# Performance work log

Measured on AMD Instinct MI355X. Metric: run time of the kernel, lower is better.

The kernel has to match this reference:

```python
import jax, jax.numpy as jnp
import numpy as np

GROUPS = 32
EPS = 1e-5


def setup_inputs() -> dict:
    key = jax.random.key(0)
    ks = jax.random.split(key, 6)
    B, H, W, C = 2, 64, 64, 512
    wscale = 0.02  # keep logits in a sane range for softmax
    return {
        "x": jax.random.normal(ks[0], (B, H, W, C), dtype=jnp.float32),
        "gamma": jnp.ones((C,), jnp.float32),
        "beta": jnp.zeros((C,), jnp.float32),
        "wq": jax.random.normal(ks[1], (C, C), dtype=jnp.float32) * wscale,
        "bq": jnp.zeros((C,), jnp.float32),
        "wk": jax.random.normal(ks[2], (C, C), dtype=jnp.float32) * wscale,
        "bk": jnp.zeros((C,), jnp.float32),
        "wv": jax.random.normal(ks[3], (C, C), dtype=jnp.float32) * wscale,
        "bv": jnp.zeros((C,), jnp.float32),
        "wp": jax.random.normal(ks[4], (C, C), dtype=jnp.float32) * wscale,
        "bp": jnp.zeros((C,), jnp.float32),
    }


def _group_norm(x, gamma, beta):
    B, H, W, C = x.shape
    xg = x.reshape(B, H, W, GROUPS, C // GROUPS)
    mean = xg.mean(axis=(1, 2, 4), keepdims=True)
    var = xg.var(axis=(1, 2, 4), keepdims=True)
    xn = ((xg - mean) * jax.lax.rsqrt(var + EPS)).reshape(B, H, W, C)
    return xn * gamma + beta


def reference(x, gamma, beta, wq, bq, wk, bk, wv, bv, wp, bp):
    B, H, W, C = x.shape
    xn = _group_norm(x, gamma, beta)
    # 1x1 convs == per-pixel linear layers
    q = (xn @ wq + bq).reshape(B, H * W, C)
    k = (xn @ wk + bk).reshape(B, H * W, C)
    v = (xn @ wv + bv).reshape(B, H * W, C)
    scale = C ** (-0.5)
    attn = jax.nn.softmax(jnp.einsum("bqc,bkc->bqk", q, k) * scale, axis=-1)
    out = jnp.einsum("bqk,bkc->bqc", attn, v).reshape(B, H, W, C)
    return (out @ wp + bp) + x
```

## Files before the change

### kernel.cpp

```cpp
#include <hip/hip_runtime.h>


typedef __bf16 bf16_t;
typedef __bf16 bf16x8 __attribute__((ext_vector_type(8)));
typedef __bf16 bf16x4 __attribute__((ext_vector_type(4)));
typedef float  f32x4  __attribute__((ext_vector_type(4)));

__device__ __forceinline__ bf16x8 ld8(const bf16_t* p) {
    return *reinterpret_cast<const bf16x8*>(p);
}
__device__ __forceinline__ f32x4 mfma16(bf16x8 a, bf16x8 b, f32x4 c) {
    return __builtin_amdgcn_mfma_f32_16x16x32_bf16(a, b, c, 0, 0, 0);
}
__device__ __forceinline__ void gload16(const bf16_t* gp, bf16_t* lp) {
    __builtin_amdgcn_global_load_lds(
        (const __attribute__((address_space(1))) void*)gp,
        (__attribute__((address_space(3))) void*)lp, 16, 0, 0);
}

#define NPIX 8192
#define C512 512
#define SEQ  4096
#define QSCALE 0.044194173824159216f

__global__ __launch_bounds__(256) void gn_sum_k(const float* __restrict__ x,
                                                float* __restrict__ accum) {
    int bg    = blockIdx.x >> 3;
    int slice = blockIdx.x & 7;
    int b = bg >> 5, g = bg & 31;
    const float* xp = x + (size_t)b * SEQ * C512 + g * 16;
    float s = 0.f, s2 = 0.f;
    #pragma unroll
    for (int pp = 0; pp < 2; pp++) {
        int p = slice * 512 + pp * 256 + threadIdx.x;
        const float4* q = reinterpret_cast<const float4*>(xp + (size_t)p * C512);
        #pragma unroll
        for (int i = 0; i < 4; i++) {
            float4 v = q[i];
            s  += v.x + v.y + v.z + v.w;
            s2 += v.x*v.x + v.y*v.y + v.z*v.z + v.w*v.w;
        }
    }
    #pragma unroll
    for (int off = 32; off >= 1; off >>= 1) {
        s  += __shfl_down(s, off);
        s2 += __shfl_down(s2, off);
    }
    __shared__ float rs[4], rs2[4];
    int wave = threadIdx.x >> 6;
    if ((threadIdx.x & 63) == 0) { rs[wave] = s; rs2[wave] = s2; }
    __syncthreads();
    if (threadIdx.x == 0) {
        float S = rs[0] + rs[1] + rs[2] + rs[3];
        float S2 = rs2[0] + rs2[1] + rs2[2] + rs2[3];
        atomicAdd(&accum[bg * 2],     S);
        atomicAdd(&accum[bg * 2 + 1], S2);
    }
}

__global__ __launch_bounds__(256) void wt_conv_k(const float* wq, const float* wk,
                                                 const float* wv, const float* wp,
                                                 const float* bq, const float* bk,
                                                 const float* bv,
                                                 bf16_t* wqkvT, bf16_t* wpT,
                                                 float* bqkv) {
    int y = blockIdx.y;
    if (y == 4) {
        if (blockIdx.x >= 6) return;
        int i = blockIdx.x * 256 + threadIdx.x;
        float v = (i < 512) ? bq[i] * QSCALE : (i < 1024) ? bk[i - 512] : bv[i - 1024];
        bqkv[i] = v;
        return;
    }
    const float* w = (y == 0) ? wq : (y == 1) ? wk : (y == 2) ? wv : wp;
    float scale = (y == 0) ? QSCALE : 1.0f;
    int tid = blockIdx.x * 256 + threadIdx.x;
    int n = tid >> 9, k = tid & 511;
    bf16_t val = (bf16_t)(w[(size_t)k * C512 + n] * scale);
    if (y < 3) wqkvT[((size_t)y * C512 + n) * C512 + k] = val;
    else       wpT[(size_t)n * C512 + k] = val;
}

__global__ __launch_bounds__(256) void xn_k(const float* __restrict__ x,
                                            const float* __restrict__ accum,
                                            const float* __restrict__ gamma,
                                            const float* __restrict__ beta,
                                            bf16_t* __restrict__ xn) {
    size_t idx = ((size_t)blockIdx.x * 256 + threadIdx.x) * 4;
    int c = (int)(idx & 511);
    size_t pix = idx >> 9;
    int b = (int)(pix >> 12);
    int g = c >> 4;
    float sum = accum[(b * 32 + g) * 2];
    float ssq = accum[(b * 32 + g) * 2 + 1];
    float mean = sum * (1.f / 65536.f);
    float var  = ssq * (1.f / 65536.f) - mean * mean;
    float rstd = rsqrtf(var + 1e-5f);
    float4 v  = *reinterpret_cast<const float4*>(x + idx);
    float4 gm = *reinterpret_cast<const float4*>(gamma + c);
    float4 bt = *reinterpret_cast<const float4*>(beta + c);
    bf16x4 o;
    o[0] = (bf16_t)((v.x - mean) * rstd * gm.x + bt.x);
    o[1] = (bf16_t)((v.y - mean) * rstd * gm.y + bt.y);
    o[2] = (bf16_t)((v.z - mean) * rstd * gm.z + bt.z);
    o[3] = (bf16_t)((v.w - mean) * rstd * gm.w + bt.w);
    *reinterpret_cast<bf16x4*>(xn + idx) = o;
}

template <int MODE>
__global__ __launch_bounds__(256, 2) void gemm128_k(
        const bf16_t* __restrict__ Aall, const bf16_t* __restrict__ Ball,
        const float* __restrict__ bias, const float* __restrict__ resid,
        void* __restrict__ out0, void* __restrict__ out1,
        void* __restrict__ out2, void* __restrict__ out3,
        float* __restrict__ lsum) {
    constexpr int TM  = (MODE == 3) ? 64 : 128;
    constexpr int ASZ = TM * 32;
    constexpr int ACH = TM / 16;
    constexpr int CPW = (ACH + 8) / 4;
    constexpr int MI  = TM / 32;
    constexpr int SME = (MODE == 0) ? (128 * 136) : (2 * ASZ + 8192);
    __shared__ bf16_t smem[SME];

    int lane = threadIdx.x & 63;
    int w    = threadIdx.x >> 6;
    int wr   = w >> 1, wc = w & 1;
    int lrow = lane & 15, quad = lane >> 4;

    const bf16_t* A  = Aall;
    const bf16_t* A1 = (MODE == 3) ? (const bf16_t*)out1 : nullptr;
    const bf16_t* B  = Ball;
    size_t lda = 512, ldb = 512;
    int ksteps = (MODE == 3) ? 32 : 16;

    int bm = blockIdx.x * TM, bn = blockIdx.y * 128;

    auto stage = [&](int buf, int ks) {
        const bf16_t* Ap = (MODE == 3 && ks >= 16) ? A1 : A;
        size_t k0 = (size_t)(MODE == 3 ? (ks & 15) : ks) * 32;
        #pragma unroll
        for (int ii = 0; ii < CPW; ii++) {
            int c = w * CPW + ii;
            if (c < ACH) {
                const bf16_t* gpA = Ap + (size_t)(bm + c * 16 + lrow) * lda + k0 + quad * 8;
                gload16(gpA, &smem[buf * ASZ + c * 512]);
            } else {
                int cb = c - ACH;
                const bf16_t* gpB = B + (size_t)(bn + cb * 16 + lrow) * ldb + k0 + quad * 8;
                gload16(gpB, &smem[2 * ASZ + buf * 4096 + cb * 512]);
            }
        }
    };

    f32x4 acc[MI][4] = {};

    stage(0, 0);

    for (int ks = 0; ks < ksteps; ks++) {
        int cur = ks & 1;
        __syncthreads();
        if (ks + 1 < ksteps) stage(1 - cur, ks + 1);

        const bf16_t* al = &smem[cur * ASZ + (wr * MI) * 512];
        const bf16_t* bl = &smem[2 * ASZ + cur * 4096 + (wc * 4) * 512];
        bf16x8 af[MI], bf[4];
        #pragma unroll
        for (int m = 0; m < MI; m++) af[m] = ld8(al + m * 512 + lane * 8);
        #pragma unroll
        for (int n = 0; n < 4; n++) bf[n] = ld8(bl + n * 512 + lane * 8);
        #pragma unroll
        for (int m = 0; m < MI; m++)
            #pragma unroll
            for (int n = 0; n < 4; n++)
                acc[m][n] = mfma16(af[m], bf[n], acc[m][n]);
    }

    if (MODE == 0 && bn >= 1024) {
        __syncthreads();
        #pragma unroll
        for (int m = 0; m < MI; m++) {
            int lr0 = wr * 64 + m * 16 + quad * 4;
            #pragma unroll
            for (int n = 0; n < 4; n++) {
                int lc = wc * 64 + n * 16 + lrow;
                float bsc = bias[bn + lc];
                #pragma unroll
                for (int i = 0; i < 4; i++)
                    smem[(lr0 + i) * 136 + lc] = (bf16_t)(acc[m][n][i] + bsc);
            }
        }
        __syncthreads();
        int cc = threadIdx.x >> 1, sh = threadIdx.x & 1;
        int b = bm >> 12, s0 = (bm & 4095) + sh * 64;
        bf16_t* VTp = (bf16_t*)out2 +
                      ((size_t)(b * C512 + (bn - 1024) + cc)) * SEQ + s0;
        #pragma unroll
        for (int j = 0; j < 8; j++) {
            bf16x8 v;
            #pragma unroll
            for (int e = 0; e < 8; e++)
                v[e] = smem[(sh * 64 + j * 8 + e) * 136 + cc];
            *reinterpret_cast<bf16x8*>(VTp + j * 8) = v;
        }
        return;
    }
    #pragma unroll
    for (int m = 0; m < MI; m++) {
        int rowb = bm + wr * (TM / 2) + m * 16 + quad * 4;
        #pragma unroll
        for (int n = 0; n < 4; n++) {
            int col = bn + wc * 64 + n * 16 + lrow;
            #pragma unroll
            for (int i = 0; i < 4; i++) {
                int row = rowb + i;
                float v = acc[m][n][i];
                if (MODE == 0) {
                    int seg = col >> 9, c = col & 511;
                    bf16_t val = (bf16_t)(v + bias[col]);
                    if (seg == 0) ((bf16_t*)out0)[(size_t)row * C512 + c] = val;
                    else          ((bf16_t*)out1)[(size_t)row * C512 + c] = val;
                } else {
                    size_t idx = (size_t)row * C512 + col;
                    float inv = 1.0f / lsum[row];
                    ((float*)out0)[idx] = v * inv + bias[col] + resid[idx];
                }
            }
        }
    }
}

__global__ __launch_bounds__(512, 1) void fattn_k(
        const bf16_t* __restrict__ Q, const bf16_t* __restrict__ K,
        const bf16_t* __restrict__ VT, bf16_t* __restrict__ Op0,
        bf16_t* __restrict__ Op1, float* __restrict__ lsum) {
    __shared__ bf16_t Kl[2][32 * 512];
    __shared__ bf16_t Vl[2][512 * 32];
    __shared__ bf16_t Pl[64 * 32];

    int bid = blockIdx.x;
    int xcd = bid & 7, loc = bid >> 3;
    int b   = (xcd >> 1) & 1;
    int kv  = xcd & 1;
    int q0  = ((xcd >> 2) * 32 + loc) * 64;
    int key0 = kv * 2048;

    const bf16_t* Qb = Q  + (size_t)b * SEQ * C512;
    const bf16_t* Kb = K  + (size_t)b * SEQ * C512;
    const bf16_t* Vb = VT + (size_t)b * C512 * SEQ;
    bf16_t* Op = kv ? Op1 : Op0;

    int lane = threadIdx.x & 63;
    int w    = threadIdx.x >> 6;
    int lrow = lane & 15, quad = lane >> 4;
    int qt = w & 3, kt = w >> 2;

    bf16x8 qf[16];
    const bf16_t* qp = Qb + (size_t)(q0 + qt * 16 + lrow) * C512 + quad * 8;
    #pragma unroll
    for (int ks = 0; ks < 16; ks++) qf[ks] = ld8(qp + ks * 32);

    auto stage = [&](int buf, int t) {
        #pragma unroll
        for (int ii = 0; ii < 8; ii++) {
            int cc = w * 8 + ii;
            if (cc < 32) {
                int ks = cc >> 1, ktc = cc & 1;
                const bf16_t* gp = Kb +
                    (size_t)(key0 + t * 32 + ktc * 16 + lrow) * C512 + ks * 32 + quad * 8;
                gload16(gp, &Kl[buf][cc * 512]);
            } else {
                int ct = cc - 32;
                const bf16_t* gp = Vb +
                    (size_t)(ct * 16 + lrow) * SEQ + key0 + t * 32 + quad * 8;
                gload16(gp, &Vl[buf][ct * 512]);
            }
        }
    };

    f32x4 oacc[4][4] = {};
    float rs[4] = {0.f, 0.f, 0.f, 0.f};

    stage(0, 0);

    for (int t = 0; t < 64; t++) {
        int cur = t & 1;
        __syncthreads();
        if (t < 63) stage(1 - cur, t + 1);

        f32x4 sa = {0.f, 0.f, 0.f, 0.f};
        #pragma unroll
        for (int ks = 0; ks < 16; ks++) {
            bf16x8 bf = ld8(&Kl[cur][(ks * 2 + kt) * 512 + lane * 8]);
            sa = mfma16(qf[ks], bf, sa);
        }
        #pragma unroll
        for (int i = 0; i < 4; i++) {
            float p = __expf(fminf(sa[i], 20.0f));
            rs[i] += p;
            int off = qt * 512 + (quad * 4 + i) * 8 +
                      (kt * 2 + (lrow >> 3)) * 128 + (lrow & 7);
            Pl[off] = (bf16_t)p;
        }
        asm volatile("s_waitcnt lgkmcnt(0)" ::: "memory");
        __builtin_amdgcn_s_barrier();
        __builtin_amdgcn_sched_barrier(0);

        bf16x8 pa[4];
        #pragma unroll
        for (int m = 0; m < 4; m++) pa[m] = ld8(&Pl[m * 512 + lane * 8]);
        #pragma unroll
        for (int n = 0; n < 4; n++) {
            bf16x8 vf = ld8(&Vl[cur][(w * 4 + n) * 512 + lane * 8]);
            #pragma unroll
            for (int m = 0; m < 4; m++)
                oacc[m][n] = mfma16(pa[m], vf, oacc[m][n]);
        }
    }

    #pragma unroll
    for (int i = 0; i < 4; i++) {
        float r = rs[i];
        r += __shfl_xor(r, 1);
        r += __shfl_xor(r, 2);
        r += __shfl_xor(r, 4);
        r += __shfl_xor(r, 8);
        if (lrow == 0)
            atomicAdd(&lsum[(size_t)b * SEQ + q0 + qt * 16 + quad * 4 + i], r);
    }

    #pragma unroll
    for (int m = 0; m < 4; m++) {
        int row = q0 + m * 16 + quad * 4;
        #pragma unroll
        for (int n = 0; n < 4; n++) {
            int col = w * 64 + n * 16 + lrow;
            #pragma unroll
            for (int i = 0; i < 4; i++)
                Op[((size_t)b * SEQ + row + i) * C512 + col] = (bf16_t)oacc[m][n][i];
        }
    }
}

extern "C" void kernel_launch(void* const* d_in, const int* in_sizes, int n_in,
                              void* d_out, int out_size, void* d_ws, size_t ws_size,
                              hipStream_t stream) {
    const float* x     = (const float*)d_in[0];
    const float* gamma = (const float*)d_in[1];
    const float* beta  = (const float*)d_in[2];
    const float* wq = (const float*)d_in[3];  const float* bq = (const float*)d_in[4];
    const float* wk = (const float*)d_in[5];  const float* bk = (const float*)d_in[6];
    const float* wv = (const float*)d_in[7];  const float* bv = (const float*)d_in[8];
    const float* wp = (const float*)d_in[9];  const float* bp = (const float*)d_in[10];
    float* out = (float*)d_out;

    char* ws = (char*)d_ws;
    size_t off = 0;
    float*  bqkv   = (float*)(ws + off);   off += 1536 * sizeof(float);
    float*  lsum   = (float*)(ws + off);   off += (size_t)NPIX * sizeof(float);
    float*  accum  = (float*)(ws + off);   off += 128 * sizeof(float);
    bf16_t* xn     = (bf16_t*)(ws + off);  off += (size_t)NPIX * C512 * 2;
    bf16_t* wqkvT  = (bf16_t*)(ws + off);  off += (size_t)3 * C512 * C512 * 2;
    bf16_t* wpT    = (bf16_t*)(ws + off);  off += (size_t)C512 * C512 * 2;
    bf16_t* Qb     = (bf16_t*)(ws + off);  off += (size_t)NPIX * C512 * 2;
    bf16_t* Kb     = (bf16_t*)(ws + off);  off += (size_t)NPIX * C512 * 2;
    bf16_t* VTb    = (bf16_t*)(ws + off);  off += (size_t)NPIX * C512 * 2;
    bf16_t* Op0    = (bf16_t*)(ws + off);  off += (size_t)NPIX * C512 * 2;
    bf16_t* Op1    = (bf16_t*)(ws + off);  off += (size_t)NPIX * C512 * 2;

    hipMemsetAsync(lsum, 0, (size_t)(NPIX + 128) * sizeof(float), stream);

    gn_sum_k<<<512, 256, 0, stream>>>(x, accum);
    wt_conv_k<<<dim3(1024, 5), 256, 0, stream>>>(wq, wk, wv, wp, bq, bk, bv,
                                                 wqkvT, wpT, bqkv);
    xn_k<<<4096, 256, 0, stream>>>(x, accum, gamma, beta, xn);

    gemm128_k<0><<<dim3(64, 12, 1), 256, 0, stream>>>(
        xn, wqkvT, bqkv, nullptr, Qb, Kb, VTb, nullptr, nullptr);

    fattn_k<<<256, 512, 0, stream>>>(Qb, Kb, VTb, Op0, Op1, lsum);

    gemm128_k<3><<<dim3(128, 4, 1), 256, 0, stream>>>(
        Op0, wpT, bp, x, out, Op1, nullptr, nullptr, lsum);
}
```

Measured before the change: 303.0 us.

## Use 128-query tiles with 4-way KV split in flash attention

The attention kernel now runs 1024 threads per block on 128-query tiles. It splits the key range four ways instead of two, so each K/V tile staged in shared memory is reused across twice as many queries. The four partial outputs go to separate buffers, and the projection GEMM sums them by extending its K loop to 64 steps over the four buffers. This cuts redundant K/V loads from global memory. In exchange it adds more partial-output traffic, two extra workspace buffers, and higher register pressure at 1024 threads per block.

```diff
diff --git a/kernel.cpp b/kernel.cpp
--- a/kernel.cpp
+++ b/kernel.cpp
@@ -128,15 +128,19 @@
     int lrow = lane & 15, quad = lane >> 4;
 
     const bf16_t* A  = Aall;
-    const bf16_t* A1 = (MODE == 3) ? (const bf16_t*)out1 : nullptr;
     const bf16_t* B  = Ball;
     size_t lda = 512, ldb = 512;
-    int ksteps = (MODE == 3) ? 32 : 16;
+    int ksteps = (MODE == 3) ? 64 : 16;
 
     int bm = blockIdx.x * TM, bn = blockIdx.y * 128;
 
     auto stage = [&](int buf, int ks) {
-        const bf16_t* Ap = (MODE == 3 && ks >= 16) ? A1 : A;
+        const bf16_t* Ap = A;
+        if (MODE == 3) {
+            int sel = ks >> 4;
+            Ap = (sel == 0) ? A : (sel == 1) ? (const bf16_t*)out1
+               : (sel == 2) ? (const bf16_t*)out2 : (const bf16_t*)out3;
+        }
         size_t k0 = (size_t)(MODE == 3 ? (ks & 15) : ks) * 32;
         #pragma unroll
         for (int ii = 0; ii < CPW; ii++) {
@@ -229,40 +233,42 @@
     }
 }
 
-__global__ __launch_bounds__(512, 1) void fattn_k(
+__global__ __launch_bounds__(1024, 1) void fattn_k(
         const bf16_t* __restrict__ Q, const bf16_t* __restrict__ K,
         const bf16_t* __restrict__ VT, bf16_t* __restrict__ Op0,
-        bf16_t* __restrict__ Op1, float* __restrict__ lsum) {
+        bf16_t* __restrict__ Op1, bf16_t* __restrict__ Op2,
+        bf16_t* __restrict__ Op3, float* __restrict__ lsum) {
     __shared__ bf16_t Kl[2][32 * 512];
     __shared__ bf16_t Vl[2][512 * 32];
-    __shared__ bf16_t Pl[64 * 32];
+    __shared__ bf16_t Pl[128 * 32];
 
     int bid = blockIdx.x;
     int xcd = bid & 7, loc = bid >> 3;
-    int b   = (xcd >> 1) & 1;
-    int kv  = xcd & 1;
-    int q0  = ((xcd >> 2) * 32 + loc) * 64;
-    int key0 = kv * 2048;
+    int b   = xcd & 1;
+    int kvq = xcd >> 1;
+    int q0  = loc * 128;
+    int key0 = kvq * 1024;
 
     const bf16_t* Qb = Q  + (size_t)b * SEQ * C512;
     const bf16_t* Kb = K  + (size_t)b * SEQ * C512;
     const bf16_t* Vb = VT + (size_t)b * C512 * SEQ;
-    bf16_t* Op = kv ? Op1 : Op0;
+    bf16_t* Op = (kvq == 0) ? Op0 : (kvq == 1) ? Op1 : (kvq == 2) ? Op2 : Op3;
 
     int lane = threadIdx.x & 63;
     int w    = threadIdx.x >> 6;
     int lrow = lane & 15, quad = lane >> 4;
-    int qt = w & 3, kt = w >> 2;
+    int qh = w >> 1, kt = w & 1;
+    int mq = w & 3, nh = w >> 2;
 
     bf16x8 qf[16];
-    const bf16_t* qp = Qb + (size_t)(q0 + qt * 16 + lrow) * C512 + quad * 8;
+    const bf16_t* qp = Qb + (size_t)(q0 + qh * 16 + lrow) * C512 + quad * 8;
     #pragma unroll
     for (int ks = 0; ks < 16; ks++) qf[ks] = ld8(qp + ks * 32);
 
     auto stage = [&](int buf, int t) {
         #pragma unroll
-        for (int ii = 0; ii < 8; ii++) {
-            int cc = w * 8 + ii;
+        for (int ii = 0; ii < 4; ii++) {
+            int cc = w * 4 + ii;
             if (cc < 32) {
                 int ks = cc >> 1, ktc = cc & 1;
                 const bf16_t* gp = Kb +
@@ -277,27 +283,27 @@
         }
     };
 
-    f32x4 oacc[4][4] = {};
+    f32x4 oacc[2][8] = {};
     float rs[4] = {0.f, 0.f, 0.f, 0.f};
 
     stage(0, 0);
 
-    for (int t = 0; t < 64; t++) {
+    for (int t = 0; t < 32; t++) {
         int cur = t & 1;
         __syncthreads();
-        if (t < 63) stage(1 - cur, t + 1);
+        if (t < 31) stage(1 - cur, t + 1);
 
         f32x4 sa = {0.f, 0.f, 0.f, 0.f};
         #pragma unroll
         for (int ks = 0; ks < 16; ks++) {
-            bf16x8 bf = ld8(&Kl[cur][(ks * 2 + kt) * 512 + lane * 8]);
-            sa = mfma16(qf[ks], bf, sa);
+            bf16x8 kf = ld8(&Kl[cur][(ks * 2 + kt) * 512 + lane * 8]);
+            sa = mfma16(qf[ks], kf, sa);
         }
         #pragma unroll
         for (int i = 0; i < 4; i++) {
             float p = __expf(fminf(sa[i], 20.0f));
             rs[i] += p;
-            int off = qt * 512 + (quad * 4 + i) * 8 +
+            int off = qh * 512 + (quad * 4 + i) * 8 +
                       (kt * 2 + (lrow >> 3)) * 128 + (lrow & 7);
             Pl[off] = (bf16_t)p;
         }
@@ -305,15 +311,14 @@
         __builtin_amdgcn_s_barrier();
         __builtin_amdgcn_sched_barrier(0);
 
-        bf16x8 pa[4];
-        #pragma unroll
-        for (int m = 0; m < 4; m++) pa[m] = ld8(&Pl[m * 512 + lane * 8]);
-        #pragma unroll
-        for (int n = 0; n < 4; n++) {
-            bf16x8 vf = ld8(&Vl[cur][(w * 4 + n) * 512 + lane * 8]);
-            #pragma unroll
-            for (int m = 0; m < 4; m++)
-                oacc[m][n] = mfma16(pa[m], vf, oacc[m][n]);
+        bf16x8 pa[2];
+        pa[0] = ld8(&Pl[(mq * 2 + 0) * 512 + lane * 8]);
+        pa[1] = ld8(&Pl[(mq * 2 + 1) * 512 + lane * 8]);
+        #pragma unroll
+        for (int n = 0; n < 8; n++) {
+            bf16x8 vf = ld8(&Vl[cur][(nh * 8 + n) * 512 + lane * 8]);
+            oacc[0][n] = mfma16(pa[0], vf, oacc[0][n]);
+            oacc[1][n] = mfma16(pa[1], vf, oacc[1][n]);
         }
     }
 
@@ -325,18 +330,18 @@
         r += __shfl_xor(r, 4);
         r += __shfl_xor(r, 8);
         if (lrow == 0)
-            atomicAdd(&lsum[(size_t)b * SEQ + q0 + qt * 16 + quad * 4 + i], r);
-    }
-
-    #pragma unroll
-    for (int m = 0; m < 4; m++) {
-        int row = q0 + m * 16 + quad * 4;
-        #pragma unroll
-        for (int n = 0; n < 4; n++) {
-            int col = w * 64 + n * 16 + lrow;
+            atomicAdd(&lsum[(size_t)b * SEQ + q0 + qh * 16 + quad * 4 + i], r);
+    }
+
+    #pragma unroll
+    for (int j = 0; j < 2; j++) {
+        int row = q0 + (mq * 2 + j) * 16 + quad * 4;
+        #pragma unroll
+        for (int n = 0; n < 8; n++) {
+            int col = nh * 128 + n * 16 + lrow;
             #pragma unroll
             for (int i = 0; i < 4; i++)
-                Op[((size_t)b * SEQ + row + i) * C512 + col] = (bf16_t)oacc[m][n][i];
+                Op[((size_t)b * SEQ + row + i) * C512 + col] = (bf16_t)oacc[j][n][i];
         }
     }
 }
@@ -366,6 +371,8 @@
     bf16_t* VTb    = (bf16_t*)(ws + off);  off += (size_t)NPIX * C512 * 2;
     bf16_t* Op0    = (bf16_t*)(ws + off);  off += (size_t)NPIX * C512 * 2;
     bf16_t* Op1    = (bf16_t*)(ws + off);  off += (size_t)NPIX * C512 * 2;
+    bf16_t* Op2    = (bf16_t*)(ws + off);  off += (size_t)NPIX * C512 * 2;
+    bf16_t* Op3    = (bf16_t*)(ws + off);  off += (size_t)NPIX * C512 * 2;
 
     hipMemsetAsync(lsum, 0, (size_t)(NPIX + 128) * sizeof(float), stream);
 
@@ -377,8 +384,8 @@
     gemm128_k<0><<<dim3(64, 12, 1), 256, 0, stream>>>(
         xn, wqkvT, bqkv, nullptr, Qb, Kb, VTb, nullptr, nullptr);
 
-    fattn_k<<<256, 512, 0, stream>>>(Qb, Kb, VTb, Op0, Op1, lsum);
+    fattn_k<<<256, 1024, 0, stream>>>(Qb, Kb, VTb, Op0, Op1, Op2, Op3, lsum);
 
     gemm128_k<3><<<dim3(128, 4, 1), 256, 0, stream>>>(
-        Op0, wpT, bp, x, out, Op1, nullptr, nullptr, lsum);
-}
+        Op0, wpT, bp, x, out, Op1, Op2, Op3, lsum);
+}
```

New measurement: 526.9 us. 73.9% more time.

## Split attention keys four ways and load V fragments directly from global

Applied to the files above, without the earlier changes.

The attention kernel now splits the key range into four chunks instead of two. The grid doubles to 512 blocks, each covering a quarter of the keys for a 64-query tile, and writes its own partial-output buffer. The V tile is no longer staged through LDS: each wave loads its V fragments straight from global memory into registers at the start of each step, which shrinks LDS use and removes the V staging traffic. The output projection GEMM now reduces over four partial buffers (K=2048), which adds extra memory traffic and GEMM work, and the uncached direct V loads may expose latency.

```diff
diff --git a/kernel.cpp b/kernel.cpp
--- a/kernel.cpp
+++ b/kernel.cpp
@@ -128,15 +128,19 @@
     int lrow = lane & 15, quad = lane >> 4;
 
     const bf16_t* A  = Aall;
-    const bf16_t* A1 = (MODE == 3) ? (const bf16_t*)out1 : nullptr;
     const bf16_t* B  = Ball;
     size_t lda = 512, ldb = 512;
-    int ksteps = (MODE == 3) ? 32 : 16;
+    int ksteps = (MODE == 3) ? 64 : 16;
 
     int bm = blockIdx.x * TM, bn = blockIdx.y * 128;
 
     auto stage = [&](int buf, int ks) {
-        const bf16_t* Ap = (MODE == 3 && ks >= 16) ? A1 : A;
+        const bf16_t* Ap = A;
+        if (MODE == 3) {
+            int sel = ks >> 4;
+            Ap = (sel == 0) ? A : (sel == 1) ? (const bf16_t*)out1
+               : (sel == 2) ? (const bf16_t*)out2 : (const bf16_t*)out3;
+        }
         size_t k0 = (size_t)(MODE == 3 ? (ks & 15) : ks) * 32;
         #pragma unroll
         for (int ii = 0; ii < CPW; ii++) {
@@ -232,22 +236,22 @@
 __global__ __launch_bounds__(512, 1) void fattn_k(
         const bf16_t* __restrict__ Q, const bf16_t* __restrict__ K,
         const bf16_t* __restrict__ VT, bf16_t* __restrict__ Op0,
-        bf16_t* __restrict__ Op1, float* __restrict__ lsum) {
+        bf16_t* __restrict__ Op1, bf16_t* __restrict__ Op2,
+        bf16_t* __restrict__ Op3, float* __restrict__ lsum) {
     __shared__ bf16_t Kl[2][32 * 512];
-    __shared__ bf16_t Vl[2][512 * 32];
     __shared__ bf16_t Pl[64 * 32];
 
     int bid = blockIdx.x;
     int xcd = bid & 7, loc = bid >> 3;
-    int b   = (xcd >> 1) & 1;
-    int kv  = xcd & 1;
-    int q0  = ((xcd >> 2) * 32 + loc) * 64;
-    int key0 = kv * 2048;
+    int b   = xcd & 1;
+    int kvq = xcd >> 1;
+    int q0  = loc * 64;
+    int key0 = kvq * 1024;
 
     const bf16_t* Qb = Q  + (size_t)b * SEQ * C512;
     const bf16_t* Kb = K  + (size_t)b * SEQ * C512;
     const bf16_t* Vb = VT + (size_t)b * C512 * SEQ;
-    bf16_t* Op = kv ? Op1 : Op0;
+    bf16_t* Op = (kvq == 0) ? Op0 : (kvq == 1) ? Op1 : (kvq == 2) ? Op2 : Op3;
 
     int lane = threadIdx.x & 63;
     int w    = threadIdx.x >> 6;
@@ -259,39 +263,40 @@
     #pragma unroll
     for (int ks = 0; ks < 16; ks++) qf[ks] = ld8(qp + ks * 32);
 
-    auto stage = [&](int buf, int t) {
-        #pragma unroll
-        for (int ii = 0; ii < 8; ii++) {
-            int cc = w * 8 + ii;
-            if (cc < 32) {
-                int ks = cc >> 1, ktc = cc & 1;
-                const bf16_t* gp = Kb +
-                    (size_t)(key0 + t * 32 + ktc * 16 + lrow) * C512 + ks * 32 + quad * 8;
-                gload16(gp, &Kl[buf][cc * 512]);
-            } else {
-                int ct = cc - 32;
-                const bf16_t* gp = Vb +
-                    (size_t)(ct * 16 + lrow) * SEQ + key0 + t * 32 + quad * 8;
-                gload16(gp, &Vl[buf][ct * 512]);
-            }
+    auto stageK = [&](int buf, int t) {
+        #pragma unroll
+        for (int ii = 0; ii < 4; ii++) {
+            int cc = w * 4 + ii;
+            int ks = cc >> 1, ktc = cc & 1;
+            const bf16_t* gp = Kb +
+                (size_t)(key0 + t * 32 + ktc * 16 + lrow) * C512 + ks * 32 + quad * 8;
+            gload16(gp, &Kl[buf][cc * 512]);
         }
     };
+    const bf16_t* vbase = Vb + (size_t)(w * 64 + lrow) * SEQ + key0 + quad * 8;
 
     f32x4 oacc[4][4] = {};
     float rs[4] = {0.f, 0.f, 0.f, 0.f};
 
-    stage(0, 0);
-
-    for (int t = 0; t < 64; t++) {
+    stageK(0, 0);
+
+    for (int t = 0; t < 32; t++) {
         int cur = t & 1;
         __syncthreads();
-        if (t < 63) stage(1 - cur, t + 1);
+
+        bf16x8 vf[4];
+        const bf16_t* vp = vbase + (size_t)t * 32;
+        #pragma unroll
+        for (int n = 0; n < 4; n++) vf[n] = ld8(vp + (size_t)(n * 16) * SEQ);
+        __builtin_amdgcn_sched_barrier(0);
+
+        if (t < 31) stageK(1 - cur, t + 1);
 
         f32x4 sa = {0.f, 0.f, 0.f, 0.f};
         #pragma unroll
         for (int ks = 0; ks < 16; ks++) {
-            bf16x8 bf = ld8(&Kl[cur][(ks * 2 + kt) * 512 + lane * 8]);
-            sa = mfma16(qf[ks], bf, sa);
+            bf16x8 kf = ld8(&Kl[cur][(ks * 2 + kt) * 512 + lane * 8]);
+            sa = mfma16(qf[ks], kf, sa);
         }
         #pragma unroll
         for (int i = 0; i < 4; i++) {
@@ -309,12 +314,10 @@
         #pragma unroll
         for (int m = 0; m < 4; m++) pa[m] = ld8(&Pl[m * 512 + lane * 8]);
         #pragma unroll
-        for (int n = 0; n < 4; n++) {
-            bf16x8 vf = ld8(&Vl[cur][(w * 4 + n) * 512 + lane * 8]);
+        for (int n = 0; n < 4; n++)
             #pragma unroll
             for (int m = 0; m < 4; m++)
-                oacc[m][n] = mfma16(pa[m], vf, oacc[m][n]);
-        }
+                oacc[m][n] = mfma16(pa[m], vf[n], oacc[m][n]);
     }
 
     #pragma unroll
@@ -366,6 +369,8 @@
     bf16_t* VTb    = (bf16_t*)(ws + off);  off += (size_t)NPIX * C512 * 2;
     bf16_t* Op0    = (bf16_t*)(ws + off);  off += (size_t)NPIX * C512 * 2;
     bf16_t* Op1    = (bf16_t*)(ws + off);  off += (size_t)NPIX * C512 * 2;
+    bf16_t* Op2    = (bf16_t*)(ws + off);  off += (size_t)NPIX * C512 * 2;
+    bf16_t* Op3    = (bf16_t*)(ws + off);  off += (size_t)NPIX * C512 * 2;
 
     hipMemsetAsync(lsum, 0, (size_t)(NPIX + 128) * sizeof(float), stream);
 
@@ -377,8 +382,8 @@
     gemm128_k<0><<<dim3(64, 12, 1), 256, 0, stream>>>(
         xn, wqkvT, bqkv, nullptr, Qb, Kb, VTb, nullptr, nullptr);
 
-    fattn_k<<<256, 512, 0, stream>>>(Qb, Kb, VTb, Op0, Op1, lsum);
+    fattn_k<<<512, 512, 0, stream>>>(Qb, Kb, VTb, Op0, Op1, Op2, Op3, lsum);
 
     gemm128_k<3><<<dim3(128, 4, 1), 256, 0, stream>>>(
-        Op0, wpT, bp, x, out, Op1, nullptr, nullptr, lsum);
-}
+        Op0, wpT, bp, x, out, Op1, Op2, Op3, lsum);
+}
```

After: 364.8 us. 20.4% more time.
